# Performance work log

Measured on AMD Instinct MI355X. Metric: run time of the kernel, lower is better.

Reference implementation:

```python
import jax, jax.numpy as jnp
import numpy as np

RADIUS = 96
B, IN, OUT, DYN, K = 32, 32, 32, 16, 7


def hex_neighbor_indices(radius):
    # Hex grid cells in axial coords: |i|<r, |k|<r, |i-k|<r, lexicographic order.
    cells = [(i, k) for i in range(-radius + 1, radius)
             for k in range(-radius + 1, radius) if abs(i - k) < radius]
    idx = {c: n for n, c in enumerate(cells)}
    offsets = [(-1, -1), (-1, 0), (0, -1), (0, 0), (0, 1), (1, 0), (1, 1)]
    nbr = np.full((len(offsets), len(cells)), -1, np.int32)
    for n, (i, k) in enumerate(cells):
        for o, (di, dk) in enumerate(offsets):
            nbr[o, n] = idx.get((i + di, k + dk), -1)
    return nbr


def setup_inputs() -> dict:
    key = jax.random.key(0)
    k1, k2, k3, k4 = jax.random.split(key, 4)
    nbr = hex_neighbor_indices(RADIUS)          # (7, N), -1 = invalid neighbor
    N = nbr.shape[1]                            # 3r^2-3r+1 = 27361
    return {
        "grid": jax.random.normal(k1, (B, N, IN), jnp.float32),
        "dyn": jax.random.normal(k2, (B, K, DYN), jnp.float32),
        "neighbor_idx": jnp.asarray(nbr),
        "Wdyn": jax.random.normal(k3, (K, DYN, IN, OUT), jnp.float32) * 0.05,
        "Wstatic": jax.random.normal(k4, (K, IN, OUT), jnp.float32) * 0.05,
        "bias": jnp.zeros((OUT,), jnp.float32),
    }


def reference(grid, dyn, neighbor_idx, Wdyn, Wstatic, bias):
    # grid: (B, N, in), dyn: (B, 7, dyn_dim), neighbor_idx: (7, N)
    mask = neighbor_idx >= 0                      # (7, N)
    safe = jnp.where(mask, neighbor_idx, 0)
    gathered = jnp.take(grid, safe, axis=1)       # (B, 7, N, in)
    gathered = gathered * mask[None, :, :, None].astype(grid.dtype)
    # dynamic per-neighbor kernel: einsum('bd,dio->bio') for each k
    dyn_kernel = jnp.einsum('bkd,kdio->bkio', dyn, Wdyn)      # (B, 7, in, out)
    dyn_proj = jnp.einsum('bkni,bkio->bno', gathered, dyn_kernel)
    static_proj = jnp.einsum('bkni,kio->bno', gathered, Wstatic)
    return dyn_proj + static_proj + bias          # (B, N, out); shrink=False, no activation
```

## Files before the change

### kernel.cpp

```cpp
#include <hip/hip_runtime.h>
#include <hip/hip_bf16.h>

typedef __attribute__((ext_vector_type(8))) short short8;
typedef __attribute__((ext_vector_type(4))) float f32x4;

static constexpr int IN = 32, OUT = 32, DYNDIM = 16, KNBR = 7;
static constexpr int ROWS = 512;
static constexpr int PAD  = 192;
static constexpr int WIN  = ROWS + 2 * PAD;
static constexpr int LROW = 36;
static constexpr int NT   = 512;

__device__ inline unsigned short f2bf(float f) {
    unsigned u = __builtin_bit_cast(unsigned, f);
    unsigned r = (u + 0x7fffu + ((u >> 16) & 1u)) >> 16;
    return (unsigned short)r;
}

__device__ inline unsigned cvtpk(float lo, float hi) {
    unsigned r;
    asm("v_cvt_pk_bf16_f32 %0, %1, %2" : "=v"(r) : "v"(lo), "v"(hi));
    return r;
}

__global__ void pack_weights(const float* __restrict__ dyn,
                             const float* __restrict__ Wdyn,
                             const float* __restrict__ Wstat,
                             unsigned short* __restrict__ Wp)
{
    int bk = blockIdx.x;
    int k  = bk % KNBR;
    __shared__ float dsh[DYNDIM];
    if (threadIdx.x < DYNDIM)
        dsh[threadIdx.x] = dyn[(size_t)bk * DYNDIM + threadIdx.x];
    __syncthreads();

    for (int e = threadIdx.x; e < IN * OUT; e += blockDim.x) {
        int i = e >> 5, o = e & 31;
        float acc = Wstat[((size_t)k * IN + i) * OUT + o];
        const float* wd = Wdyn + (((size_t)k * DYNDIM) * IN + i) * OUT + o;
#pragma unroll
        for (int d = 0; d < DYNDIM; ++d)
            acc += dsh[d] * wd[(size_t)d * IN * OUT];
        int ch = o & 1, cc = o >> 1, g = i >> 3, j = i & 7;
        Wp[(((size_t)bk * 2 + ch) * 64 + (g * 16 + cc)) * 8 + j] = f2bf(acc);
    }
}

__global__ __launch_bounds__(NT, 4) void hexconv_fused(
    const float* __restrict__ grid,
    const int* __restrict__ nbr,
    const unsigned short* __restrict__ Wp,
    const float* __restrict__ bias,
    float* __restrict__ out,
    int N)
{
    __shared__ unsigned short glds[(WIN + 1) * LROW];

    const int nwgx = gridDim.x;
    const int nwg  = nwgx * gridDim.y;
    int orig = blockIdx.x + nwgx * blockIdx.y;
    int wg = orig;
    if ((nwg & 7) == 0) {
        int cpx = nwg >> 3;
        wg = (orig & 7) * cpx + (orig >> 3);
    }
    const int bx = wg % nwgx;
    const int b  = wg / nwgx;

    const int base   = bx * ROWS;
    const int win_lo = base - PAD;
    const size_t gbase = (size_t)b * N * 32;

    const int lane = threadIdx.x & 63;
    const int w    = threadIdx.x >> 6;
    const int g    = lane >> 4;
    const int c    = lane & 15;
    const int wbase = base + w * 64;

    const unsigned short* wpb = Wp + (size_t)b * KNBR * 1024;
    short8 bw[KNBR][2];
#pragma unroll
    for (int kk = 0; kk < KNBR; ++kk)
#pragma unroll
        for (int ch = 0; ch < 2; ++ch)
            bw[kk][ch] = *(const short8*)(wpb + ((size_t)(kk * 2 + ch) * 64 + lane) * 8);

    int idxc[KNBR];
    {
        const int n0 = wbase + c;
        const bool v = (n0 < N);
#pragma unroll
        for (int kk = 0; kk < KNBR; ++kk) {
            if (kk == 3) idxc[kk] = v ? n0 : -1;
            else         idxc[kk] = v ? nbr[(size_t)kk * N + n0] : -1;
        }
    }

    if (threadIdx.x < 18)
        ((unsigned*)(glds + WIN * LROW))[threadIdx.x] = 0;

    const bool interior = (win_lo >= 0) && (win_lo + WIN <= N);
    if (interior) {
#pragma unroll
        for (int it = 0; it < (WIN * 4) / NT; ++it) {
            int e = threadIdx.x + it * NT;
            int row = e >> 2, seg = e & 3;
            const float* gp = grid + gbase + (size_t)(win_lo + row) * 32 + seg * 8;
            float4 x0 = *(const float4*)gp;
            float4 x1 = *(const float4*)(gp + 4);
            uint4 vv;
            vv.x = cvtpk(x0.x, x0.y);
            vv.y = cvtpk(x0.z, x0.w);
            vv.z = cvtpk(x1.x, x1.y);
            vv.w = cvtpk(x1.z, x1.w);
            *(uint4*)(glds + row * LROW + seg * 8) = vv;
        }
    } else {
#pragma unroll
        for (int it = 0; it < (WIN * 4) / NT; ++it) {
            int e = threadIdx.x + it * NT;
            int row = e >> 2, seg = e & 3;
            int gr = win_lo + row;
            if (gr >= 0 && gr < N) {
                const float* gp = grid + gbase + (size_t)gr * 32 + seg * 8;
                float4 x0 = *(const float4*)gp;
                float4 x1 = *(const float4*)(gp + 4);
                uint4 vv;
                vv.x = cvtpk(x0.x, x0.y);
                vv.y = cvtpk(x0.z, x0.w);
                vv.z = cvtpk(x1.x, x1.y);
                vv.w = cvtpk(x1.z, x1.w);
                *(uint4*)(glds + row * LROW + seg * 8) = vv;
            }
        }
    }
    __syncthreads();

    const float bc0 = bias[2 * c];
    const float bc1 = bias[2 * c + 1];

#pragma unroll
    for (int t = 0; t < 4; ++t) {
        int idxn[KNBR];
        if (t < 3) {
            const int n1 = wbase + (t + 1) * 16 + c;
            const bool v = (n1 < N);
#pragma unroll
            for (int kk = 0; kk < KNBR; ++kk) {
                if (kk == 3) idxn[kk] = v ? n1 : -1;
                else         idxn[kk] = v ? nbr[(size_t)kk * N + n1] : -1;
            }
        }

        f32x4 acc0 = {0.f, 0.f, 0.f, 0.f};
        f32x4 acc1 = {0.f, 0.f, 0.f, 0.f};
#pragma unroll
        for (int kk = 0; kk < KNBR; ++kk) {
            int off = (idxc[kk] < 0) ? WIN : (idxc[kk] - win_lo);
            short8 a = *(const short8*)(glds + (size_t)off * LROW + g * 8);
            acc0 = __builtin_amdgcn_mfma_f32_16x16x32_bf16(a, bw[kk][0], acc0, 0, 0, 0);
            acc1 = __builtin_amdgcn_mfma_f32_16x16x32_bf16(a, bw[kk][1], acc1, 0, 0, 0);
        }

        const int row_base = wbase + t * 16 + g * 4;
#pragma unroll
        for (int r = 0; r < 4; ++r) {
            int row = row_base + r;
            if (row < N) {
                float* op = out + gbase + (size_t)row * 32;
                float2 v2;
                v2.x = acc0[r] + bc0;
                v2.y = acc1[r] + bc1;
                __builtin_nontemporal_store(
                    __builtin_bit_cast(unsigned long long, v2),
                    (unsigned long long*)(op + 2 * c));
            }
        }

        if (t < 3) {
#pragma unroll
            for (int kk = 0; kk < KNBR; ++kk) idxc[kk] = idxn[kk];
        }
    }
}

extern "C" void kernel_launch(void* const* d_in, const int* in_sizes, int n_in,
                              void* d_out, int out_size, void* d_ws, size_t ws_size,
                              hipStream_t stream)
{
    const float* grid  = (const float*)d_in[0];
    const float* dyn   = (const float*)d_in[1];
    const int*   nbr   = (const int*)d_in[2];
    const float* Wdyn  = (const float*)d_in[3];
    const float* Wstat = (const float*)d_in[4];
    const float* bias  = (const float*)d_in[5];
    float* out = (float*)d_out;

    const int N = in_sizes[2] / KNBR;
    const int B = in_sizes[0] / (N * IN);

    unsigned short* Wp = (unsigned short*)d_ws;
    pack_weights<<<B * KNBR, 256, 0, stream>>>(dyn, Wdyn, Wstat, Wp);

    dim3 grd((N + ROWS - 1) / ROWS, B);
    hexconv_fused<<<grd, NT, 0, stream>>>(grid, nbr, Wp, bias, out, N);
}
```

Before: 57.15 us.

## Split window load into two chunks and overlap second chunk with first tile compute

The shared-memory window fill for interior blocks is split. The first 512 rows are loaded and converted before the barrier, while the remaining rows are fetched into registers and written to LDS only after the first 16-row tile per wave has been computed. Row assignment per wave changes from a contiguous 64-row strip to interleaved 16-row tiles with stride 128, so the first tile only needs rows inside the first chunk. This is meant to hide part of the global load latency behind MFMA work, at the cost of extra registers for the staged float4 values and a second barrier.

```diff
diff --git a/kernel.cpp b/kernel.cpp
--- a/kernel.cpp
+++ b/kernel.cpp
@@ -8,6 +8,8 @@
 static constexpr int ROWS = 512;
 static constexpr int PAD  = 192;
 static constexpr int WIN  = ROWS + 2 * PAD;
+static constexpr int CHA  = 512;
+static constexpr int CH2  = WIN - CHA;
 static constexpr int LROW = 36;
 static constexpr int NT   = 512;
 
@@ -76,7 +78,6 @@
     const int w    = threadIdx.x >> 6;
     const int g    = lane >> 4;
     const int c    = lane & 15;
-    const int wbase = base + w * 64;
 
     const unsigned short* wpb = Wp + (size_t)b * KNBR * 1024;
     short8 bw[KNBR][2];
@@ -88,7 +89,7 @@
 
     int idxc[KNBR];
     {
-        const int n0 = wbase + c;
+        const int n0 = base + w * 16 + c;
         const bool v = (n0 < N);
 #pragma unroll
         for (int kk = 0; kk < KNBR; ++kk) {
@@ -101,9 +102,11 @@
         ((unsigned*)(glds + WIN * LROW))[threadIdx.x] = 0;
 
     const bool interior = (win_lo >= 0) && (win_lo + WIN <= N);
+    float4 c2lo[3], c2hi[3];
+
     if (interior) {
 #pragma unroll
-        for (int it = 0; it < (WIN * 4) / NT; ++it) {
+        for (int it = 0; it < (CHA * 4) / NT; ++it) {
             int e = threadIdx.x + it * NT;
             int row = e >> 2, seg = e & 3;
             const float* gp = grid + gbase + (size_t)(win_lo + row) * 32 + seg * 8;
@@ -115,6 +118,14 @@
             vv.z = cvtpk(x1.x, x1.y);
             vv.w = cvtpk(x1.z, x1.w);
             *(uint4*)(glds + row * LROW + seg * 8) = vv;
+        }
+#pragma unroll
+        for (int u = 0; u < (CH2 * 4) / NT; ++u) {
+            int e = threadIdx.x + u * NT;
+            int row = CHA + (e >> 2), seg = e & 3;
+            const float* gp = grid + gbase + (size_t)(win_lo + row) * 32 + seg * 8;
+            c2lo[u] = *(const float4*)gp;
+            c2hi[u] = *(const float4*)(gp + 4);
         }
     } else {
 #pragma unroll
@@ -140,19 +151,18 @@
     const float bc0 = bias[2 * c];
     const float bc1 = bias[2 * c + 1];
 
-#pragma unroll
-    for (int t = 0; t < 4; ++t) {
-        int idxn[KNBR];
-        if (t < 3) {
-            const int n1 = wbase + (t + 1) * 16 + c;
-            const bool v = (n1 < N);
-#pragma unroll
-            for (int kk = 0; kk < KNBR; ++kk) {
-                if (kk == 3) idxn[kk] = v ? n1 : -1;
-                else         idxn[kk] = v ? nbr[(size_t)kk * N + n1] : -1;
-            }
-        }
-
+    int idxn[KNBR];
+    {
+        const int n1 = base + 128 + w * 16 + c;
+        const bool v = (n1 < N);
+#pragma unroll
+        for (int kk = 0; kk < KNBR; ++kk) {
+            if (kk == 3) idxn[kk] = v ? n1 : -1;
+            else         idxn[kk] = v ? nbr[(size_t)kk * N + n1] : -1;
+        }
+    }
+
+    {
         f32x4 acc0 = {0.f, 0.f, 0.f, 0.f};
         f32x4 acc1 = {0.f, 0.f, 0.f, 0.f};
 #pragma unroll
@@ -162,8 +172,7 @@
             acc0 = __builtin_amdgcn_mfma_f32_16x16x32_bf16(a, bw[kk][0], acc0, 0, 0, 0);
             acc1 = __builtin_amdgcn_mfma_f32_16x16x32_bf16(a, bw[kk][1], acc1, 0, 0, 0);
         }
-
-        const int row_base = wbase + t * 16 + g * 4;
+        const int row_base = base + w * 16 + g * 4;
 #pragma unroll
         for (int r = 0; r < 4; ++r) {
             int row = row_base + r;
@@ -177,10 +186,60 @@
                     (unsigned long long*)(op + 2 * c));
             }
         }
-
+    }
+
+    if (interior) {
+#pragma unroll
+        for (int u = 0; u < (CH2 * 4) / NT; ++u) {
+            int e = threadIdx.x + u * NT;
+            int row = CHA + (e >> 2), seg = e & 3;
+            uint4 vv;
+            vv.x = cvtpk(c2lo[u].x, c2lo[u].y);
+            vv.y = cvtpk(c2lo[u].z, c2lo[u].w);
+            vv.z = cvtpk(c2hi[u].x, c2hi[u].y);
+            vv.w = cvtpk(c2hi[u].z, c2hi[u].w);
+            *(uint4*)(glds + row * LROW + seg * 8) = vv;
+        }
+    }
+    __syncthreads();
+
+#pragma unroll
+    for (int t = 1; t < 4; ++t) {
+#pragma unroll
+        for (int kk = 0; kk < KNBR; ++kk) idxc[kk] = idxn[kk];
         if (t < 3) {
-#pragma unroll
-            for (int kk = 0; kk < KNBR; ++kk) idxc[kk] = idxn[kk];
+            const int n1 = base + (t + 1) * 128 + w * 16 + c;
+            const bool v = (n1 < N);
+#pragma unroll
+            for (int kk = 0; kk < KNBR; ++kk) {
+                if (kk == 3) idxn[kk] = v ? n1 : -1;
+                else         idxn[kk] = v ? nbr[(size_t)kk * N + n1] : -1;
+            }
+        }
+
+        f32x4 acc0 = {0.f, 0.f, 0.f, 0.f};
+        f32x4 acc1 = {0.f, 0.f, 0.f, 0.f};
+#pragma unroll
+        for (int kk = 0; kk < KNBR; ++kk) {
+            int off = (idxc[kk] < 0) ? WIN : (idxc[kk] - win_lo);
+            short8 a = *(const short8*)(glds + (size_t)off * LROW + g * 8);
+            acc0 = __builtin_amdgcn_mfma_f32_16x16x32_bf16(a, bw[kk][0], acc0, 0, 0, 0);
+            acc1 = __builtin_amdgcn_mfma_f32_16x16x32_bf16(a, bw[kk][1], acc1, 0, 0, 0);
+        }
+
+        const int row_base = base + t * 128 + w * 16 + g * 4;
+#pragma unroll
+        for (int r = 0; r < 4; ++r) {
+            int row = row_base + r;
+            if (row < N) {
+                float* op = out + gbase + (size_t)row * 32;
+                float2 v2;
+                v2.x = acc0[r] + bc0;
+                v2.y = acc1[r] + bc1;
+                __builtin_nontemporal_store(
+                    __builtin_bit_cast(unsigned long long, v2),
+                    (unsigned long long*)(op + 2 * c));
+            }
         }
     }
 }
```

Measured after the change: 56.27 us. About the same (-1.5%).

## Add persistent double-buffered kernel looping over batch groups with prefetch

Applied to the files above, without the earlier changes.

Adds a new kernel in which each workgroup processes 8 batch items for one spatial tile. The next batch's grid window is prefetched into registers while the current batch's MFMAs run, then written into a second LDS buffer. Neighbor offsets are computed once per block and reused across all batches, removing repeated index loads. The cost is fewer blocks (the grid shrinks by a factor of 8), twice the LDS, and a lower occupancy bound, which may reduce latency hiding and parallelism.

```diff
diff --git a/kernel.cpp b/kernel.cpp
--- a/kernel.cpp
+++ b/kernel.cpp
@@ -9,14 +9,16 @@
 static constexpr int PAD  = 192;
 static constexpr int WIN  = ROWS + 2 * PAD;
 static constexpr int LROW = 36;
+static constexpr int BUFR = WIN + 1;
 static constexpr int NT   = 512;
+static constexpr int NBGRP = 8;
+static constexpr int LDS_BYTES = 2 * BUFR * LROW * 2;
 
 __device__ inline unsigned short f2bf(float f) {
     unsigned u = __builtin_bit_cast(unsigned, f);
     unsigned r = (u + 0x7fffu + ((u >> 16) & 1u)) >> 16;
     return (unsigned short)r;
 }
-
 __device__ inline unsigned cvtpk(float lo, float hi) {
     unsigned r;
     asm("v_cvt_pk_bf16_f32 %0, %1, %2" : "=v"(r) : "v"(lo), "v"(hi));
@@ -47,35 +49,164 @@
     }
 }
 
+struct StepArgs {
+    const float* grid; const unsigned short* Wp; const float* bias; float* out;
+    const unsigned short* glds; int N; int win_lo; int wbase; int lane, g, c;
+    float bc0, bc1; int srow0, sseg;
+};
+
+template<int RB, int WB>
+__device__ __forceinline__ void pipe_step(const StepArgs& A, unsigned short* glds,
+                                          const int off[4][KNBR], int b, bool pre)
+{
+    const unsigned short* wpb = A.Wp + (size_t)b * KNBR * 1024;
+    short8 bw[KNBR][2];
+#pragma unroll
+    for (int kk = 0; kk < KNBR; ++kk)
+#pragma unroll
+        for (int ch = 0; ch < 2; ++ch)
+            bw[kk][ch] = *(const short8*)(wpb + ((size_t)(kk * 2 + ch) * 64 + A.lane) * 8);
+
+    float4 hlo[7], hhi[7];
+    if (pre) {
+        const float* gb = A.grid + (size_t)(b + 1) * A.N * 32;
+#pragma unroll
+        for (int it = 0; it < 7; ++it) {
+            hlo[it] = make_float4(0.f, 0.f, 0.f, 0.f);
+            hhi[it] = make_float4(0.f, 0.f, 0.f, 0.f);
+            int gr = A.win_lo + A.srow0 + it * 128;
+            if (gr >= 0 && gr < A.N) {
+                const float* gp = gb + (size_t)gr * 32 + A.sseg * 8;
+                hlo[it] = *(const float4*)gp;
+                hhi[it] = *(const float4*)(gp + 4);
+            }
+        }
+    }
+
+    const size_t obase = (size_t)b * A.N * 32;
+#pragma unroll
+    for (int t = 0; t < 4; ++t) {
+        f32x4 a0 = {0.f, 0.f, 0.f, 0.f};
+        f32x4 a1 = {0.f, 0.f, 0.f, 0.f};
+#pragma unroll
+        for (int kk = 0; kk < KNBR; ++kk) {
+            const short8 av = *(const short8*)(glds + RB * BUFR * LROW +
+                                               (size_t)off[t][kk] * LROW + A.g * 8);
+            a0 = __builtin_amdgcn_mfma_f32_16x16x32_bf16(av, bw[kk][0], a0, 0, 0, 0);
+            a1 = __builtin_amdgcn_mfma_f32_16x16x32_bf16(av, bw[kk][1], a1, 0, 0, 0);
+        }
+        const int row_base = A.wbase + t * 16 + A.g * 4;
+#pragma unroll
+        for (int r = 0; r < 4; ++r) {
+            int row = row_base + r;
+            if (row < A.N) {
+                float* op = A.out + obase + (size_t)row * 32;
+                float2 v2; v2.x = a0[r] + A.bc0; v2.y = a1[r] + A.bc1;
+                __builtin_nontemporal_store(
+                    __builtin_bit_cast(unsigned long long, v2),
+                    (unsigned long long*)(op + 2 * A.c));
+            }
+        }
+    }
+
+    if (pre) {
+#pragma unroll
+        for (int it = 0; it < 7; ++it) {
+            uint4 vv;
+            vv.x = cvtpk(hlo[it].x, hlo[it].y);
+            vv.y = cvtpk(hlo[it].z, hlo[it].w);
+            vv.z = cvtpk(hhi[it].x, hhi[it].y);
+            vv.w = cvtpk(hhi[it].z, hhi[it].w);
+            *(uint4*)(glds + WB * BUFR * LROW +
+                      (A.srow0 + it * 128) * LROW + A.sseg * 8) = vv;
+        }
+    }
+    __syncthreads();
+}
+
+__global__ __launch_bounds__(NT, 2) void hexconv_pipe(
+    const float* __restrict__ grid, const int* __restrict__ nbr,
+    const unsigned short* __restrict__ Wp, const float* __restrict__ bias,
+    float* __restrict__ out, int N)
+{
+    extern __shared__ unsigned short glds[];
+
+    const int nwg = gridDim.x;
+    int orig = blockIdx.x, wg = orig;
+    if ((nwg & 7) == 0) { int cpx = nwg >> 3; wg = (orig & 7) * cpx + (orig >> 3); }
+    const int NBX = (N + ROWS - 1) / ROWS;
+    const int bx = wg % NBX;
+    const int b0 = (wg / NBX) * NBGRP;
+
+    const int base = bx * ROWS, win_lo = base - PAD;
+    const int lane = threadIdx.x & 63, w = threadIdx.x >> 6;
+    const int g = lane >> 4, c = lane & 15;
+    const int wbase = base + w * 64;
+    const int srow0 = threadIdx.x >> 2, sseg = threadIdx.x & 3;
+
+    int off[4][KNBR];
+#pragma unroll
+    for (int t = 0; t < 4; ++t) {
+        int n0 = wbase + t * 16 + c;
+        bool v = (n0 < N);
+#pragma unroll
+        for (int kk = 0; kk < KNBR; ++kk) {
+            int id = (kk == 3) ? (v ? n0 : -1)
+                               : (v ? nbr[(size_t)kk * N + n0] : -1);
+            off[t][kk] = (id < 0) ? WIN : (id - win_lo);
+        }
+    }
+
+    if (threadIdx.x < 18) {
+        ((unsigned*)(glds + WIN * LROW))[threadIdx.x] = 0;
+        ((unsigned*)(glds + (BUFR + WIN) * LROW))[threadIdx.x] = 0;
+    }
+
+    {
+        const float* gb = grid + (size_t)b0 * N * 32;
+#pragma unroll
+        for (int it = 0; it < 7; ++it) {
+            float4 x0 = make_float4(0.f, 0.f, 0.f, 0.f);
+            float4 x1 = make_float4(0.f, 0.f, 0.f, 0.f);
+            int gr = win_lo + srow0 + it * 128;
+            if (gr >= 0 && gr < N) {
+                const float* gp = gb + (size_t)gr * 32 + sseg * 8;
+                x0 = *(const float4*)gp; x1 = *(const float4*)(gp + 4);
+            }
+            uint4 vv;
+            vv.x = cvtpk(x0.x, x0.y); vv.y = cvtpk(x0.z, x0.w);
+            vv.z = cvtpk(x1.x, x1.y); vv.w = cvtpk(x1.z, x1.w);
+            *(uint4*)(glds + (srow0 + it * 128) * LROW + sseg * 8) = vv;
+        }
+    }
+    __syncthreads();
+
+    StepArgs A{grid, Wp, bias, out, glds, N, win_lo, wbase, lane, g, c,
+               bias[2 * c], bias[2 * c + 1], srow0, sseg};
+
+#pragma unroll 1
+    for (int jp = 0; jp < NBGRP / 2; ++jp) {
+        int j0 = 2 * jp;
+        pipe_step<0, 1>(A, glds, off, b0 + j0, true);
+        pipe_step<1, 0>(A, glds, off, b0 + j0 + 1, (j0 + 1) < NBGRP - 1);
+    }
+}
+
 __global__ __launch_bounds__(NT, 4) void hexconv_fused(
-    const float* __restrict__ grid,
-    const int* __restrict__ nbr,
-    const unsigned short* __restrict__ Wp,
-    const float* __restrict__ bias,
-    float* __restrict__ out,
-    int N)
-{
-    __shared__ unsigned short glds[(WIN + 1) * LROW];
-
+    const float* __restrict__ grid, const int* __restrict__ nbr,
+    const unsigned short* __restrict__ Wp, const float* __restrict__ bias,
+    float* __restrict__ out, int N)
+{
+    __shared__ unsigned short slds[BUFR * LROW];
     const int nwgx = gridDim.x;
     const int nwg  = nwgx * gridDim.y;
-    int orig = blockIdx.x + nwgx * blockIdx.y;
-    int wg = orig;
-    if ((nwg & 7) == 0) {
-        int cpx = nwg >> 3;
-        wg = (orig & 7) * cpx + (orig >> 3);
-    }
-    const int bx = wg % nwgx;
-    const int b  = wg / nwgx;
-
-    const int base   = bx * ROWS;
-    const int win_lo = base - PAD;
+    int orig = blockIdx.x + nwgx * blockIdx.y, wg = orig;
+    if ((nwg & 7) == 0) { int cpx = nwg >> 3; wg = (orig & 7) * cpx + (orig >> 3); }
+    const int bx = wg % nwgx, b = wg / nwgx;
+    const int base = bx * ROWS, win_lo = base - PAD;
     const size_t gbase = (size_t)b * N * 32;
-
-    const int lane = threadIdx.x & 63;
-    const int w    = threadIdx.x >> 6;
-    const int g    = lane >> 4;
-    const int c    = lane & 15;
+    const int lane = threadIdx.x & 63, w = threadIdx.x >> 6;
+    const int g = lane >> 4, c = lane & 15;
     const int wbase = base + w * 64;
 
     const unsigned short* wpb = Wp + (size_t)b * KNBR * 1024;
@@ -86,101 +217,54 @@
         for (int ch = 0; ch < 2; ++ch)
             bw[kk][ch] = *(const short8*)(wpb + ((size_t)(kk * 2 + ch) * 64 + lane) * 8);
 
-    int idxc[KNBR];
-    {
-        const int n0 = wbase + c;
-        const bool v = (n0 < N);
+    int off[4][KNBR];
+#pragma unroll
+    for (int t = 0; t < 4; ++t) {
+        int n0 = wbase + t * 16 + c;
+        bool v = (n0 < N);
 #pragma unroll
         for (int kk = 0; kk < KNBR; ++kk) {
-            if (kk == 3) idxc[kk] = v ? n0 : -1;
-            else         idxc[kk] = v ? nbr[(size_t)kk * N + n0] : -1;
-        }
-    }
-
+            int id = (kk == 3) ? (v ? n0 : -1) : (v ? nbr[(size_t)kk * N + n0] : -1);
+            off[t][kk] = (id < 0) ? WIN : (id - win_lo);
+        }
+    }
     if (threadIdx.x < 18)
-        ((unsigned*)(glds + WIN * LROW))[threadIdx.x] = 0;
-
-    const bool interior = (win_lo >= 0) && (win_lo + WIN <= N);
-    if (interior) {
-#pragma unroll
-        for (int it = 0; it < (WIN * 4) / NT; ++it) {
-            int e = threadIdx.x + it * NT;
-            int row = e >> 2, seg = e & 3;
-            const float* gp = grid + gbase + (size_t)(win_lo + row) * 32 + seg * 8;
-            float4 x0 = *(const float4*)gp;
-            float4 x1 = *(const float4*)(gp + 4);
+        ((unsigned*)(slds + WIN * LROW))[threadIdx.x] = 0;
+
+    for (int e = threadIdx.x; e < WIN * 4; e += NT) {
+        int row = e >> 2, seg = e & 3, gr = win_lo + row;
+        if (gr >= 0 && gr < N) {
+            const float* gp = grid + gbase + (size_t)gr * 32 + seg * 8;
+            float4 x0 = *(const float4*)gp, x1 = *(const float4*)(gp + 4);
             uint4 vv;
-            vv.x = cvtpk(x0.x, x0.y);
-            vv.y = cvtpk(x0.z, x0.w);
-            vv.z = cvtpk(x1.x, x1.y);
-            vv.w = cvtpk(x1.z, x1.w);
-            *(uint4*)(glds + row * LROW + seg * 8) = vv;
-        }
-    } else {
-#pragma unroll
-        for (int it = 0; it < (WIN * 4) / NT; ++it) {
-            int e = threadIdx.x + it * NT;
-            int row = e >> 2, seg = e & 3;
-            int gr = win_lo + row;
-            if (gr >= 0 && gr < N) {
-                const float* gp = grid + gbase + (size_t)gr * 32 + seg * 8;
-                float4 x0 = *(const float4*)gp;
-                float4 x1 = *(const float4*)(gp + 4);
-                uint4 vv;
-                vv.x = cvtpk(x0.x, x0.y);
-                vv.y = cvtpk(x0.z, x0.w);
-                vv.z = cvtpk(x1.x, x1.y);
-                vv.w = cvtpk(x1.z, x1.w);
-                *(uint4*)(glds + row * LROW + seg * 8) = vv;
-            }
+            vv.x = cvtpk(x0.x, x0.y); vv.y = cvtpk(x0.z, x0.w);
+            vv.z = cvtpk(x1.x, x1.y); vv.w = cvtpk(x1.z, x1.w);
+            *(uint4*)(slds + row * LROW + seg * 8) = vv;
         }
     }
     __syncthreads();
 
-    const float bc0 = bias[2 * c];
-    const float bc1 = bias[2 * c + 1];
-
+    const float bc0 = bias[2 * c], bc1 = bias[2 * c + 1];
 #pragma unroll
     for (int t = 0; t < 4; ++t) {
-        int idxn[KNBR];
-        if (t < 3) {
-            const int n1 = wbase + (t + 1) * 16 + c;
-            const bool v = (n1 < N);
-#pragma unroll
-            for (int kk = 0; kk < KNBR; ++kk) {
-                if (kk == 3) idxn[kk] = v ? n1 : -1;
-                else         idxn[kk] = v ? nbr[(size_t)kk * N + n1] : -1;
-            }
-        }
-
-        f32x4 acc0 = {0.f, 0.f, 0.f, 0.f};
-        f32x4 acc1 = {0.f, 0.f, 0.f, 0.f};
+        f32x4 a0 = {0.f, 0.f, 0.f, 0.f}, a1 = {0.f, 0.f, 0.f, 0.f};
 #pragma unroll
         for (int kk = 0; kk < KNBR; ++kk) {
-            int off = (idxc[kk] < 0) ? WIN : (idxc[kk] - win_lo);
-            short8 a = *(const short8*)(glds + (size_t)off * LROW + g * 8);
-            acc0 = __builtin_amdgcn_mfma_f32_16x16x32_bf16(a, bw[kk][0], acc0, 0, 0, 0);
-            acc1 = __builtin_amdgcn_mfma_f32_16x16x32_bf16(a, bw[kk][1], acc1, 0, 0, 0);
-        }
-
+            short8 av = *(const short8*)(slds + (size_t)off[t][kk] * LROW + g * 8);
+            a0 = __builtin_amdgcn_mfma_f32_16x16x32_bf16(av, bw[kk][0], a0, 0, 0, 0);
+            a1 = __builtin_amdgcn_mfma_f32_16x16x32_bf16(av, bw[kk][1], a1, 0, 0, 0);
+        }
         const int row_base = wbase + t * 16 + g * 4;
 #pragma unroll
         for (int r = 0; r < 4; ++r) {
             int row = row_base + r;
             if (row < N) {
                 float* op = out + gbase + (size_t)row * 32;
-                float2 v2;
-                v2.x = acc0[r] + bc0;
-                v2.y = acc1[r] + bc1;
+                float2 v2; v2.x = a0[r] + bc0; v2.y = a1[r] + bc1;
                 __builtin_nontemporal_store(
                     __builtin_bit_cast(unsigned long long, v2),
                     (unsigned long long*)(op + 2 * c));
             }
-        }
-
-        if (t < 3) {
-#pragma unroll
-            for (int kk = 0; kk < KNBR; ++kk) idxc[kk] = idxn[kk];
         }
     }
 }
@@ -203,6 +287,18 @@
     unsigned short* Wp = (unsigned short*)d_ws;
     pack_weights<<<B * KNBR, 256, 0, stream>>>(dyn, Wdyn, Wstat, Wp);
 
-    dim3 grd((N + ROWS - 1) / ROWS, B);
-    hexconv_fused<<<grd, NT, 0, stream>>>(grid, nbr, Wp, bias, out, N);
-}
+    const int NBX = (N + ROWS - 1) / ROWS;
+    static bool attr_ok = []() {
+        return hipFuncSetAttribute((const void*)hexconv_pipe,
+                                   hipFuncAttributeMaxDynamicSharedMemorySize,
+                                   LDS_BYTES) == hipSuccess;
+    }();
+
+    if (attr_ok && (B % NBGRP) == 0) {
+        int blocks = NBX * (B / NBGRP);
+        hexconv_pipe<<<blocks, NT, LDS_BYTES, stream>>>(grid, nbr, Wp, bias, out, N);
+    } else {
+        dim3 grd(NBX, B);
+        hexconv_fused<<<grd, NT, 0, stream>>>(grid, nbr, Wp, bias, out, N);
+    }
+}
```

New measurement: 86.25 us. +50.9%, slower.
